# Kernel tuning notes

Hardware: AMD Instinct MI355X
Metric: run time of the kernel (lower is better)

The kernel has to match this reference:

```python
import jax, jax.numpy as jnp
import numpy as np

B, L, D, H, I = 4, 1024, 2048, 16, 8192
DH = D // H  # 128
EPS = 1e-6


def setup_inputs() -> dict:
    key = jax.random.key(0)
    ks = jax.random.split(key, 10)
    hidden_states = jax.random.normal(ks[0], (B, L, D), dtype=jnp.float32)
    # additive causal mask [B,1,L,L]: 0 on allowed, large negative on masked
    causal = jnp.tril(jnp.ones((L, L), dtype=bool))
    attention_mask = jnp.where(causal, 0.0, -1e9).astype(jnp.float32)
    attention_mask = jnp.broadcast_to(attention_mask[None, None], (B, 1, L, L))
    # RoPE tables [B,L,DH]
    inv_freq = 1.0 / (10000.0 ** (jnp.arange(0, DH, 2, dtype=jnp.float32) / DH))
    pos = jnp.arange(L, dtype=jnp.float32)
    freqs = pos[:, None] * inv_freq[None, :]            # [L, DH/2]
    emb = jnp.concatenate([freqs, freqs], axis=-1)       # [L, DH]
    cos = jnp.broadcast_to(jnp.cos(emb)[None], (B, L, DH)).astype(jnp.float32)
    sin = jnp.broadcast_to(jnp.sin(emb)[None], (B, L, DH)).astype(jnp.float32)
    s = 0.02
    return {
        "hidden_states": hidden_states,
        "attention_mask": attention_mask,
        "cos": cos,
        "sin": sin,
        "q_w": jax.random.normal(ks[1], (D, D), jnp.float32) * s,
        "k_w": jax.random.normal(ks[2], (D, D), jnp.float32) * s,
        "v_w": jax.random.normal(ks[3], (D, D), jnp.float32) * s,
        "o_w": jax.random.normal(ks[4], (D, D), jnp.float32) * s,
        "gate_w": jax.random.normal(ks[5], (I, D), jnp.float32) * s,
        "up_w": jax.random.normal(ks[6], (I, D), jnp.float32) * s,
        "down_w": jax.random.normal(ks[7], (D, I), jnp.float32) * s,
        "ln1_w": jnp.ones((D,), jnp.float32),
        "ln2_w": jnp.ones((D,), jnp.float32),
    }


def _rms_norm(x, w):
    var = jnp.mean(jnp.square(x), axis=-1, keepdims=True)
    return x * jax.lax.rsqrt(var + EPS) * w


def _rotate_half(x):
    x1, x2 = jnp.split(x, 2, axis=-1)
    return jnp.concatenate([-x2, x1], axis=-1)


def reference(hidden_states, attention_mask, cos, sin, q_w, k_w, v_w, o_w,
              gate_w, up_w, down_w, ln1_w, ln2_w):
    residual = hidden_states
    h = _rms_norm(hidden_states, ln1_w)                       # [B,L,D]
    # QKV projections (torch Linear: x @ W^T)
    def heads(x, w):
        return (x @ w.T).reshape(B, L, H, DH).transpose(0, 2, 1, 3)  # [B,H,L,DH]
    q, k, v = heads(h, q_w), heads(h, k_w), heads(h, v_w)
    cos_b, sin_b = cos[:, None], sin[:, None]                 # [B,1,L,DH]
    q = q * cos_b + _rotate_half(q) * sin_b
    k = k * cos_b + _rotate_half(k) * sin_b
    scores = jnp.einsum('bhqd,bhkd->bhqk', q, k) / jnp.sqrt(jnp.float32(DH))
    scores = scores + attention_mask                          # [B,H,L,L]
    attn = jax.nn.softmax(scores, axis=-1)
    ctx = jnp.einsum('bhqk,bhkd->bhqd', attn, v)              # [B,H,L,DH]
    ctx = ctx.transpose(0, 2, 1, 3).reshape(B, L, D)
    attn_out = ctx @ o_w.T
    h1 = residual + attn_out
    h2 = _rms_norm(h1, ln2_w)
    mlp = (jax.nn.silu(h2 @ gate_w.T) * (h2 @ up_w.T)) @ down_w.T
    out = h1 + mlp
    return out, attn
```

## Files before the change

### kernel.cpp

```cpp
#include <hip/hip_runtime.h>


typedef __bf16 bf16;
typedef __bf16 bf16x8 __attribute__((ext_vector_type(8)));
typedef __bf16 bf16x4 __attribute__((ext_vector_type(4)));
typedef float  f32x4  __attribute__((ext_vector_type(4)));

constexpr int   kB  = 4;
constexpr int   kL  = 1024;
constexpr int   kD  = 2048;
constexpr int   kH  = 16;
constexpr int   kI  = 8192;
constexpr int   kDH = 128;
constexpr int   kQKV = 3 * kD;
constexpr float kEps = 1e-6f;
constexpr float kScoreScale = 0.08838834764831845f;

typedef __attribute__((address_space(1))) void gvoid_t;
typedef __attribute__((address_space(3))) void lvoid_t;

__device__ __forceinline__ void gload_lds16(const void* g, void* l) {
  __builtin_amdgcn_global_load_lds((gvoid_t*)g, (lvoid_t*)l, 16, 0, 0);
}

#define ASM_VMCNT(n) asm volatile("s_waitcnt vmcnt(" #n ")" ::: "memory")

__device__ __forceinline__ void bar_raw() {
  asm volatile("" ::: "memory");
  __builtin_amdgcn_s_barrier();
  asm volatile("" ::: "memory");
}

__global__ __launch_bounds__(256) void cast_f32_bf16_kernel(
    const float* __restrict__ x, bf16* __restrict__ y, long n) {
  long i = ((long)blockIdx.x * 256 + threadIdx.x) * 4;
  long stride = (long)gridDim.x * 256 * 4;
  for (; i < n; i += stride) {
    const float4 v = *reinterpret_cast<const float4*>(x + i);
    bf16x4 o;
    o[0] = (bf16)v.x; o[1] = (bf16)v.y; o[2] = (bf16)v.z; o[3] = (bf16)v.w;
    *reinterpret_cast<bf16x4*>(y + i) = o;
  }
}

__global__ __launch_bounds__(256) void rmsnorm_kernel(
    const float* __restrict__ x, const float* __restrict__ w,
    bf16* __restrict__ out) {
  const long row = blockIdx.x;
  const float* xr = x + row * (long)kD;
  bf16* orow = out + row * (long)kD;
  const int t = threadIdx.x;

  float4 v0 = *(const float4*)(xr + t * 8);
  float4 v1 = *(const float4*)(xr + t * 8 + 4);
  float ss = v0.x * v0.x + v0.y * v0.y + v0.z * v0.z + v0.w * v0.w +
             v1.x * v1.x + v1.y * v1.y + v1.z * v1.z + v1.w * v1.w;

  __shared__ float red[4];
  for (int off = 32; off > 0; off >>= 1) ss += __shfl_down(ss, off);
  if ((t & 63) == 0) red[t >> 6] = ss;
  __syncthreads();
  const float tot = red[0] + red[1] + red[2] + red[3];
  const float rs = rsqrtf(tot / (float)kD + kEps);

  float4 w0 = *(const float4*)(w + t * 8);
  float4 w1 = *(const float4*)(w + t * 8 + 4);
  bf16x8 o;
  o[0] = (bf16)(v0.x * rs * w0.x); o[1] = (bf16)(v0.y * rs * w0.y);
  o[2] = (bf16)(v0.z * rs * w0.z); o[3] = (bf16)(v0.w * rs * w0.w);
  o[4] = (bf16)(v1.x * rs * w1.x); o[5] = (bf16)(v1.y * rs * w1.y);
  o[6] = (bf16)(v1.z * rs * w1.z); o[7] = (bf16)(v1.w * rs * w1.w);
  *(bf16x8*)(orow + t * 8) = o;
}

__global__ __launch_bounds__(256) void rope_kernel(
    bf16* __restrict__ qkv, const float* __restrict__ cosb,
    const float* __restrict__ sinb) {
  const long row = blockIdx.x;
  const float* cr = cosb + row * (long)kDH;
  const float* sr = sinb + row * (long)kDH;
  bf16* qr = qkv + row * (long)kQKV;
  bf16* kr = qr + kD;
  const int t = threadIdx.x;
#pragma unroll
  for (int it = 0; it < 4; ++it) {
    const int p = it * 256 + t;
    const int h = p >> 6, i = p & 63;
    const int i0 = h * kDH + i, i1 = i0 + 64;
    const float c0 = cr[i], s0 = sr[i], c1 = cr[i + 64], s1 = sr[i + 64];
    const float q0 = (float)qr[i0], q1 = (float)qr[i1];
    qr[i0] = (bf16)(q0 * c0 - q1 * s0);
    qr[i1] = (bf16)(q1 * c1 + q0 * s1);
    const float k0 = (float)kr[i0], k1 = (float)kr[i1];
    kr[i0] = (bf16)(k0 * c0 - k1 * s0);
    kr[i1] = (bf16)(k1 * c1 + k0 * s1);
  }
}

__global__ __launch_bounds__(256) void transpose_v_kernel(
    const bf16* __restrict__ qkv, bf16* __restrict__ vT) {
  __shared__ bf16 tile[32][33];
  const int z = blockIdx.z, b = z / kH, h = z % kH;
  const bf16* src = qkv + (long)b * kL * kQKV + 2 * kD + h * kDH;
  bf16* dst = vT + (long)z * kDH * kL;
  const int l0 = blockIdx.x * 32, d0 = blockIdx.y * 32;
  const int tx = threadIdx.x & 31, ty = threadIdx.x >> 5;
  for (int r = ty; r < 32; r += 8)
    tile[r][tx] = src[(long)(l0 + r) * kQKV + d0 + tx];
  __syncthreads();
  for (int r = ty; r < 32; r += 8)
    dst[(long)(d0 + r) * kL + l0 + tx] = tile[tx][r];
}

__global__ __launch_bounds__(256) void merge_stats_kernel(
    const float2* __restrict__ sp, float2* __restrict__ sm) {
  const int idx = blockIdx.x * 256 + threadIdx.x;
  const int row = idx & 1023;
  const int n = ((row >> 7) + 1) * 2;
  const float2* p = sp + ((long)idx << 4);
  float M = -3.0e38f;
  for (int i = 0; i < n; ++i) M = fmaxf(M, p[i].x);
  float S = 0.f;
  for (int i = 0; i < n; ++i) S += p[i].y * expf(p[i].x - M);
  sm[idx] = make_float2(M, 1.0f / S);
}

template <int EPI>
__global__ __launch_bounds__(512) void gemm256_body(
    const bf16* __restrict__ A, int lda, const bf16* __restrict__ B, int ldb,
    bf16* __restrict__ C, int ldc, const bf16* __restrict__ Ep, int lde,
    int K) {
  constexpr int NBUF = 3;
  __shared__ __align__(16) bf16 lsA[NBUF][256 * 32];
  __shared__ __align__(16) bf16 lsB[NBUF][256 * 32];

  const int t = threadIdx.x;
  const int m0 = blockIdx.x * 256, n0 = blockIdx.y * 256;
  const int wave = t >> 6, lane = t & 63;
  const int wm = (wave >> 2) * 128, wn = (wave & 3) * 64;
  const int lr = lane & 15, lg = lane >> 4;

  f32x4 acc[8][4] = {};

  auto stage = [&](int buf, int k0) {
#pragma unroll
    for (int c = 0; c < 2; ++c) {
      const int id = c * 512 + t;
      const int row = id >> 2, col = (id & 3) * 8;
      gload_lds16(A + (long)(m0 + row) * lda + k0 + col, &lsA[buf][id * 8]);
      gload_lds16(B + (long)(n0 + row) * ldb + k0 + col, &lsB[buf][id * 8]);
    }
  };

  auto compute = [&](int buf) {
    bf16x8 af[8], bfr[4];
#pragma unroll
    for (int i = 0; i < 8; ++i)
      af[i] = *(const bf16x8*)&lsA[buf][(wm + i * 16 + lr) * 32 + lg * 8];
#pragma unroll
    for (int j = 0; j < 4; ++j)
      bfr[j] = *(const bf16x8*)&lsB[buf][(wn + j * 16 + lr) * 32 + lg * 8];
#pragma unroll
    for (int i = 0; i < 8; ++i)
#pragma unroll
      for (int j = 0; j < 4; ++j)
        acc[i][j] = __builtin_amdgcn_mfma_f32_16x16x32_bf16(af[i], bfr[j],
                                                            acc[i][j], 0, 0, 0);
  };

  stage(0, 0);
  stage(1, 32);
  int cur = 0, k0 = 0;
  for (; k0 + 64 < K; k0 += 32) {
    const int nxt = cur == 2 ? 0 : cur + 1;
    const int pre = nxt == 2 ? 0 : nxt + 1;
    stage(pre, k0 + 64);
    ASM_VMCNT(8);
    bar_raw();
    compute(cur);
    bar_raw();
    cur = nxt;
  }
  ASM_VMCNT(4);
  bar_raw();
  compute(cur);
  cur = cur == 2 ? 0 : cur + 1;
  ASM_VMCNT(0);
  bar_raw();
  compute(cur);

#pragma unroll
  for (int i = 0; i < 8; ++i) {
#pragma unroll
    for (int j = 0; j < 4; ++j) {
      const int col = n0 + wn + j * 16 + lr;
#pragma unroll
      for (int r = 0; r < 4; ++r) {
        const int row = m0 + wm + i * 16 + lg * 4 + r;
        float val = acc[i][j][r];
        if constexpr (EPI == 3) {
          const float g = (float)Ep[(long)row * lde + col];
          val = (g / (1.0f + expf(-g))) * val;
        }
        C[(long)row * ldc + col] = (bf16)val;
      }
    }
  }
}

enum { EPI_NONE = 0, EPI_ADD = 1, EPI_OUTADD = 4, EPI_PASS1 = 6, EPI_PASS2 = 7 };

template <typename OutT, int EPI, bool AF32, int NF, bool CK>
__device__ __forceinline__ void gemm_body(
    const void* __restrict__ Ap, long sAo, long sAi, int lda,
    const bf16* __restrict__ Bp, long sBo, long sBi, int ldb,
    OutT* Cp, long sCo, long sCi, int ldc,
    const void* Ep, long sEo, long sEi, int lde,
    float scale, int Hdiv, int M, int N, int K) {
  constexpr int BN = 32 * NF;
  constexpr int ACH = 512;
  constexpr int BCH = BN * 4;
  static_assert((EPI != EPI_PASS1 && EPI != EPI_PASS2) || NF == 4, "pass NF=4");

  const int z = blockIdx.z;
  const int zo = z / Hdiv, zi = z % Hdiv;

  const bf16* A = nullptr;
  const float* Af = nullptr;
  if constexpr (AF32) Af = (const float*)Ap + zo * sAo + zi * sAi;
  else                A  = (const bf16*)Ap + zo * sAo + zi * sAi;
  const bf16* Bw = Bp + zo * sBo + zi * sBi;
  OutT* C = Cp + zo * sCo + zi * sCi;

  const int t = threadIdx.x;
  const int m0 = blockIdx.y * 128, n0 = blockIdx.x * BN;

  if constexpr (EPI == EPI_PASS1) {
    if (blockIdx.x > blockIdx.y) return;
  }
  if constexpr (EPI == EPI_PASS2) {
    if (blockIdx.x > blockIdx.y) {
      for (int e = t; e < 128 * 32; e += 256) {
        const int row = e >> 5, col = (e & 31) * 4;
        *(float4*)&C[(long)(m0 + row) * ldc + n0 + col] =
            make_float4(0.f, 0.f, 0.f, 0.f);
      }
      return;
    }
  }

  __shared__ __align__(16) bf16 lsA[2][128 * 32];
  __shared__ __align__(16) bf16 lsB[2][BN * 32];

  const int wave = t >> 6, lane = t & 63;
  const int wm = (wave >> 1) * 64, wn = (wave & 1) * (NF * 16);
  const int lr = lane & 15, lg = lane >> 4;

  f32x4 acc[4][NF] = {};

  auto stage = [&](int buf, int k0) {
    if constexpr (AF32) {
#pragma unroll
      for (int c = 0; c < 2; ++c) {
        const int id = c * 256 + t;
        const int row = id >> 2, col = (id & 3) * 8;
        const float* src = Af + (long)(m0 + row) * lda + k0 + col;
        const float4 u0 = *(const float4*)src;
        const float4 u1 = *(const float4*)(src + 4);
        bf16x8 wv;
        wv[0] = (bf16)u0.x; wv[1] = (bf16)u0.y; wv[2] = (bf16)u0.z; wv[3] = (bf16)u0.w;
        wv[4] = (bf16)u1.x; wv[5] = (bf16)u1.y; wv[6] = (bf16)u1.z; wv[7] = (bf16)u1.w;
        *(bf16x8*)&lsA[buf][id * 8] = wv;
        if (NF == 4 || c == 0)
          gload_lds16(Bw + (long)(n0 + row) * ldb + k0 + col, &lsB[buf][id * 8]);
      }
    } else {
#pragma unroll
      for (int c = 0; c < (ACH + BCH) / 256; ++c) {
        const int id = c * 256 + t;
        if (id < ACH) {
          const int row = id >> 2, col = (id & 3) * 8;
          gload_lds16(A + (long)(m0 + row) * lda + k0 + col, &lsA[buf][id * 8]);
        } else {
          const int fid = id - ACH;
          const int row = fid >> 2, col = (fid & 3) * 8;
          gload_lds16(Bw + (long)(n0 + row) * ldb + k0 + col, &lsB[buf][fid * 8]);
        }
      }
    }
  };

  auto compute = [&](int buf) {
    bf16x8 af[4], bfr[NF];
#pragma unroll
    for (int i = 0; i < 4; ++i)
      af[i] = *(const bf16x8*)&lsA[buf][(wm + i * 16 + lr) * 32 + lg * 8];
#pragma unroll
    for (int j = 0; j < NF; ++j)
      bfr[j] = *(const bf16x8*)&lsB[buf][(wn + j * 16 + lr) * 32 + lg * 8];
#pragma unroll
    for (int i = 0; i < 4; ++i)
#pragma unroll
      for (int j = 0; j < NF; ++j)
        acc[i][j] = __builtin_amdgcn_mfma_f32_16x16x32_bf16(af[i], bfr[j],
                                                            acc[i][j], 0, 0, 0);
  };

  const int Klim = CK ? (m0 + 128) : K;
  int cur = 0;

  if constexpr (AF32) {
    stage(0, 0);
    __syncthreads();
    for (int k0 = 0; k0 < Klim - 32; k0 += 32) {
      stage(cur ^ 1, k0 + 32);
      compute(cur);
      __syncthreads();
      cur ^= 1;
    }
    compute(cur);
  } else {
    stage(0, 0);
    for (int k0 = 0; k0 < Klim - 32; k0 += 32) {
      stage(cur ^ 1, k0 + 32);
      if constexpr (NF == 4) ASM_VMCNT(4); else ASM_VMCNT(3);
      bar_raw();
      compute(cur);
      bar_raw();
      cur ^= 1;
    }
    ASM_VMCNT(0);
    bar_raw();
    compute(cur);
  }

  if constexpr (EPI == EPI_PASS1) {
    float2* statsP = (float2*)Ep;
    const int half = wn >> 6, nt = blockIdx.x;
#pragma unroll
    for (int i = 0; i < 4; ++i) {
#pragma unroll
      for (int r = 0; r < 4; ++r) {
        const int rowg = m0 + wm + i * 16 + lg * 4 + r;
        float v[NF];
        float mx = -3.0e38f;
#pragma unroll
        for (int j = 0; j < NF; ++j) {
          const int colg = n0 + wn + j * 16 + lr;
          v[j] = acc[i][j][r] * scale + (colg > rowg ? -1.0e9f : 0.0f);
          mx = fmaxf(mx, v[j]);
        }
        for (int sh = 1; sh <= 8; sh <<= 1) mx = fmaxf(mx, __shfl_xor(mx, sh));
        float s = 0.f;
#pragma unroll
        for (int j = 0; j < NF; ++j) s += expf(v[j] - mx);
        for (int sh = 1; sh <= 8; sh <<= 1) s += __shfl_xor(s, sh);
        if (lr == 0)
          statsP[(((long)(z << 10) + rowg) << 4) + nt * 2 + half] =
              make_float2(mx, s);
      }
    }
  } else if constexpr (EPI == EPI_PASS2) {
    const float2* sm = (const float2*)Ep;
#pragma unroll
    for (int i = 0; i < 4; ++i) {
#pragma unroll
      for (int j = 0; j < NF; ++j) {
        const int colg = n0 + wn + j * 16 + lr;
#pragma unroll
        for (int r = 0; r < 4; ++r) {
          const int rowg = m0 + wm + i * 16 + lg * 4 + r;
          float p = 0.0f;
          if (colg <= rowg) {
            const float2 st = sm[(z << 10) + rowg];
            p = expf(acc[i][j][r] * scale - st.x) * st.y;
          }
          C[(long)rowg * ldc + colg] = (OutT)p;
        }
      }
    }
  } else {
    const float* Ef = (const float*)Ep;
    long ebase = 0;
    if constexpr (EPI == EPI_ADD)
      ebase = zo * sEo + zi * sEi;
#pragma unroll
    for (int i = 0; i < 4; ++i) {
#pragma unroll
      for (int j = 0; j < NF; ++j) {
        const int col = n0 + wn + j * 16 + lr;
#pragma unroll
        for (int r = 0; r < 4; ++r) {
          const int rowi = m0 + wm + i * 16 + lg * 4 + r;
          float val = acc[i][j][r] * scale;
          const long idx = (long)rowi * ldc + col;
          if constexpr (EPI == EPI_ADD)
            val += Ef[ebase + (long)rowi * lde + col];
          if constexpr (EPI == EPI_OUTADD)
            val += (float)C[idx];
          C[idx] = (OutT)val;
        }
      }
    }
  }
}

#define GEMM_ARGS                                                        \
  const void* __restrict__ Ap, long sAo, long sAi, int lda,              \
  const bf16* __restrict__ Bp, long sBo, long sBi, int ldb,              \
  void* Cp, long sCo, long sCi, int ldc,                                 \
  const void* Ep, long sEo, long sEi, int lde,                           \
  float scale, int Hdiv, int M, int N, int K
#define GEMM_PASS Ap, sAo, sAi, lda, Bp, sBo, sBi, ldb, (OUT_T*)Cp, sCo, \
  sCi, ldc, Ep, sEo, sEi, lde, scale, Hdiv, M, N, K

#define DEF_GEMM(NAME, OUT_TY, EPI_V, AF32_V, NF_V, CK_V)                \
  __global__ __launch_bounds__(256) void NAME(GEMM_ARGS) {               \
    using OUT_T = OUT_TY;                                                \
    gemm_body<OUT_T, EPI_V, AF32_V, NF_V, CK_V>(GEMM_PASS);              \
  }

DEF_GEMM(gemm_sc1,   float, EPI_PASS1,  false, 4, false)
DEF_GEMM(gemm_sc2,   float, EPI_PASS2,  false, 4, false)
DEF_GEMM(gemm_ctx,   bf16,  EPI_NONE,   true,  2, true)
DEF_GEMM(gemm_oproj, float, EPI_ADD,    false, 2, false)
DEF_GEMM(gemm_down,  float, EPI_OUTADD, false, 2, false)

extern "C" void kernel_launch(void* const* d_in, const int* in_sizes, int n_in,
                              void* d_out, int out_size, void* d_ws,
                              size_t ws_size, hipStream_t stream) {
  (void)in_sizes; (void)n_in; (void)out_size; (void)ws_size;

  const float* hidden = (const float*)d_in[0];
  const float* cosb   = (const float*)d_in[2];
  const float* sinb   = (const float*)d_in[3];
  const float* q_w    = (const float*)d_in[4];
  const float* k_w    = (const float*)d_in[5];
  const float* v_w    = (const float*)d_in[6];
  const float* o_w    = (const float*)d_in[7];
  const float* gate_w = (const float*)d_in[8];
  const float* up_w   = (const float*)d_in[9];
  const float* down_w = (const float*)d_in[10];
  const float* ln1    = (const float*)d_in[11];
  const float* ln2    = (const float*)d_in[12];

  float* out  = (float*)d_out;
  float* attn = out + (long)kB * kL * kD;

  bf16* wsb = (bf16*)d_ws;
  long off = 0;
  bf16* WQKV = wsb + off; off += 3L * kD * kD;
  bf16* WO   = wsb + off; off += (long)kD * kD;
  bf16* WBIG = wsb + off; off += (long)kI * kD;
  bf16* HBF  = wsb + off; off += (long)kB * kL * kD;
  bf16* QKV  = wsb + off; off += (long)kB * kL * kQKV;
  bf16* GBUF = wsb + off; off += (long)kB * kL * kI;

  float2* STATS_P = (float2*)HBF;
  float2* STATS_M = STATS_P + (64L * 1024 * 16);

  const long DD = (long)kD * kD;
  const long ID = (long)kI * kD;
  const int  ML = kB * kL;

  cast_f32_bf16_kernel<<<dim3((int)(DD / 1024)), 256, 0, stream>>>(q_w, WQKV, DD);
  cast_f32_bf16_kernel<<<dim3((int)(DD / 1024)), 256, 0, stream>>>(k_w, WQKV + DD, DD);
  cast_f32_bf16_kernel<<<dim3((int)(DD / 1024)), 256, 0, stream>>>(v_w, WQKV + 2 * DD, DD);
  cast_f32_bf16_kernel<<<dim3((int)(DD / 1024)), 256, 0, stream>>>(o_w, WO, DD);

  rmsnorm_kernel<<<ML, 256, 0, stream>>>(hidden, ln1, HBF);

  gemm256_body<0><<<dim3(ML / 256, kQKV / 256), 512, 0, stream>>>(
      HBF, kD, WQKV, kD, QKV, kQKV, nullptr, 0, kD);

  rope_kernel<<<ML, 256, 0, stream>>>(QKV, cosb, sinb);

  transpose_v_kernel<<<dim3(kL / 32, kDH / 32, kB * kH), 256, 0, stream>>>(QKV, GBUF);

  gemm_sc1<<<dim3(kL / 128, kL / 128, kB * kH), 256, 0, stream>>>(
      QKV, (long)kL * kQKV, kDH, kQKV,
      QKV + kD, (long)kL * kQKV, kDH, kQKV,
      attn, (long)kH * kL * kL, (long)kL * kL, kL,
      STATS_P, 0, 0, 0,
      kScoreScale, kH, kL, kL, kDH);

  merge_stats_kernel<<<256, 256, 0, stream>>>(STATS_P, STATS_M);

  gemm_sc2<<<dim3(kL / 128, kL / 128, kB * kH), 256, 0, stream>>>(
      QKV, (long)kL * kQKV, kDH, kQKV,
      QKV + kD, (long)kL * kQKV, kDH, kQKV,
      attn, (long)kH * kL * kL, (long)kL * kL, kL,
      STATS_M, 0, 0, 0,
      kScoreScale, kH, kL, kL, kDH);

  gemm_ctx<<<dim3(kDH / 64, kL / 128, kB * kH), 256, 0, stream>>>(
      attn, (long)kH * kL * kL, (long)kL * kL, kL,
      GBUF, (long)kH * kDH * kL, (long)kDH * kL, kL,
      HBF, (long)kL * kD, kDH, kD,
      nullptr, 0, 0, 0, 1.0f, kH, kL, kDH, kL);

  gemm_oproj<<<dim3(kD / 64, ML / 128, 1), 256, 0, stream>>>(
      HBF, 0, 0, kD, WO, 0, 0, kD, out, 0, 0, kD,
      hidden, 0, 0, kD, 1.0f, 1, ML, kD, kD);

  bf16* H2 = QKV;
  rmsnorm_kernel<<<ML, 256, 0, stream>>>(out, ln2, H2);

  cast_f32_bf16_kernel<<<dim3((int)(ID / 1024)), 256, 0, stream>>>(gate_w, WBIG, ID);
  gemm256_body<0><<<dim3(ML / 256, kI / 256), 512, 0, stream>>>(
      H2, kD, WBIG, kD, GBUF, kI, nullptr, 0, kD);

  cast_f32_bf16_kernel<<<dim3((int)(ID / 1024)), 256, 0, stream>>>(up_w, WBIG, ID);
  gemm256_body<3><<<dim3(ML / 256, kI / 256), 512, 0, stream>>>(
      H2, kD, WBIG, kD, GBUF, kI, GBUF, kI, kD);

  cast_f32_bf16_kernel<<<dim3((int)(ID / 1024)), 256, 0, stream>>>(down_w, WBIG, ID);
  gemm_down<<<dim3(kD / 64, ML / 128, 1), 256, 0, stream>>>(
      GBUF, 0, 0, kI, WBIG, 0, 0, kI, out, 0, 0, kD,
      nullptr, 0, 0, 0, 1.0f, 1, ML, kD, kI);
}
```

Baseline: 1.143 ms.

## Rewrite 256x256 GEMM with BK=64 XOR-swizzled LDS and phased prefetch

```diff
diff --git a/kernel.cpp b/kernel.cpp
--- a/kernel.cpp
+++ b/kernel.cpp
@@ -126,78 +126,99 @@
 }
 
 template <int EPI>
-__global__ __launch_bounds__(512) void gemm256_body(
+__global__ __launch_bounds__(512) void gemm8p(
     const bf16* __restrict__ A, int lda, const bf16* __restrict__ B, int ldb,
     bf16* __restrict__ C, int ldc, const bf16* __restrict__ Ep, int lde,
     int K) {
-  constexpr int NBUF = 3;
-  __shared__ __align__(16) bf16 lsA[NBUF][256 * 32];
-  __shared__ __align__(16) bf16 lsB[NBUF][256 * 32];
-
+  __shared__ __align__(16) bf16 ls[2][2][2][128 * 64];
   const int t = threadIdx.x;
   const int m0 = blockIdx.x * 256, n0 = blockIdx.y * 256;
   const int wave = t >> 6, lane = t & 63;
-  const int wm = (wave >> 2) * 128, wn = (wave & 3) * 64;
+  const int ah = wave >> 2;
+  const int wm = ah * 128;
+  const int wn = (wave & 3) * 64;
+  const int bh = wn >> 7;
+  const int wnr = wn & 127;
   const int lr = lane & 15, lg = lane >> 4;
 
   f32x4 acc[8][4] = {};
 
-  auto stage = [&](int buf, int k0) {
-#pragma unroll
-    for (int c = 0; c < 2; ++c) {
-      const int id = c * 512 + t;
-      const int row = id >> 2, col = (id & 3) * 8;
-      gload_lds16(A + (long)(m0 + row) * lda + k0 + col, &lsA[buf][id * 8]);
-      gload_lds16(B + (long)(n0 + row) * ldb + k0 + col, &lsB[buf][id * 8]);
+  auto stageHalf = [&](int b, int O, int h, int k0) {
+    const bf16* S = O ? B : A;
+    const int ld = O ? ldb : lda;
+    const int base = O ? n0 : m0;
+#pragma unroll
+    for (int cc = 0; cc < 2; ++cc) {
+      const int id = cc * 512 + t;
+      const int row = id >> 3, cS = id & 7;
+      const int cG = cS ^ (row & 7);
+      gload_lds16(S + (long)(base + h * 128 + row) * ld + k0 + cG * 8,
+                  (char*)&ls[b][O][h][0] + id * 16);
     }
   };
 
-  auto compute = [&](int buf) {
-    bf16x8 af[8], bfr[4];
-#pragma unroll
-    for (int i = 0; i < 8; ++i)
-      af[i] = *(const bf16x8*)&lsA[buf][(wm + i * 16 + lr) * 32 + lg * 8];
-#pragma unroll
-    for (int j = 0; j < 4; ++j)
-      bfr[j] = *(const bf16x8*)&lsB[buf][(wn + j * 16 + lr) * 32 + lg * 8];
-#pragma unroll
-    for (int i = 0; i < 8; ++i)
-#pragma unroll
-      for (int j = 0; j < 4; ++j)
-        acc[i][j] = __builtin_amdgcn_mfma_f32_16x16x32_bf16(af[i], bfr[j],
-                                                            acc[i][j], 0, 0, 0);
+  auto lread = [&](int b, int O, int h, int row, int c16) {
+    return *(const bf16x8*)((const char*)&ls[b][O][h][0] + row * 128 +
+                            ((c16 ^ (row & 7)) << 4));
   };
 
-  stage(0, 0);
-  stage(1, 32);
-  int cur = 0, k0 = 0;
-  for (; k0 + 64 < K; k0 += 32) {
-    const int nxt = cur == 2 ? 0 : cur + 1;
-    const int pre = nxt == 2 ? 0 : nxt + 1;
-    stage(pre, k0 + 64);
-    ASM_VMCNT(8);
-    bar_raw();
-    compute(cur);
-    bar_raw();
-    cur = nxt;
-  }
-  ASM_VMCNT(4);
-  bar_raw();
-  compute(cur);
-  cur = cur == 2 ? 0 : cur + 1;
-  ASM_VMCNT(0);
-  bar_raw();
-  compute(cur);
-
-#pragma unroll
-  for (int i = 0; i < 8; ++i) {
-#pragma unroll
-    for (int j = 0; j < 4; ++j) {
-      const int col = n0 + wn + j * 16 + lr;
+  const int T = K >> 6;
+  stageHalf(0, 0, 0, 0); stageHalf(0, 0, 1, 0);
+  stageHalf(0, 1, 0, 0); stageHalf(0, 1, 1, 0);
+  stageHalf(1, 1, 0, 64); stageHalf(1, 1, 1, 64);
+
+  bf16x8 bfr[2][4];
+
+  for (int w = 0; w < T; ++w) {
+    const int c = w & 1;
+    const int k1 = (w + 1) << 6, k2 = (w + 2) << 6;
+#pragma unroll
+    for (int p = 0; p < 4; ++p) {
+      bf16x8 af[2][2];
+      if (p == 0) {
+        if (w + 1 < T) { ASM_VMCNT(4); } else { ASM_VMCNT(0); }
+        bar_raw();
+#pragma unroll
+        for (int kk = 0; kk < 2; ++kk)
+#pragma unroll
+          for (int nf = 0; nf < 4; ++nf)
+            bfr[kk][nf] = lread(c, 1, bh, wnr + nf * 16 + lr, kk * 4 + lg);
+      }
+#pragma unroll
+      for (int kk = 0; kk < 2; ++kk)
+#pragma unroll
+        for (int mf = 0; mf < 2; ++mf)
+          af[kk][mf] = lread(c, 0, ah, (2 * p + mf) * 16 + lr, kk * 4 + lg);
+      if (p == 0 && w + 1 < T) stageHalf(c ^ 1, 0, 0, k1);
+      if (p == 1 && w + 1 < T) stageHalf(c ^ 1, 0, 1, k1);
+      if (p == 2 && w + 2 < T) stageHalf(c, 1, 0, k2);
+      if (p == 3 && w + 2 < T) stageHalf(c, 1, 1, k2);
+      bar_raw();
+      asm volatile("s_waitcnt lgkmcnt(0)" ::: "memory");
+      __builtin_amdgcn_sched_barrier(0);
+      __builtin_amdgcn_s_setprio(1);
+#pragma unroll
+      for (int kk = 0; kk < 2; ++kk)
+#pragma unroll
+        for (int mf = 0; mf < 2; ++mf)
+#pragma unroll
+          for (int nf = 0; nf < 4; ++nf)
+            acc[2 * p + mf][nf] = __builtin_amdgcn_mfma_f32_16x16x32_bf16(
+                af[kk][mf], bfr[kk][nf], acc[2 * p + mf][nf], 0, 0, 0);
+      __builtin_amdgcn_s_setprio(0);
+      bar_raw();
+    }
+  }
+
+#pragma unroll
+  for (int mf = 0; mf < 8; ++mf) {
+#pragma unroll
+    for (int nf = 0; nf < 4; ++nf) {
+      const int col = n0 + wn + nf * 16 + lr;
 #pragma unroll
       for (int r = 0; r < 4; ++r) {
-        const int row = m0 + wm + i * 16 + lg * 4 + r;
-        float val = acc[i][j][r];
+        const int row = m0 + wm + mf * 16 + lg * 4 + r;
+        float val = acc[mf][nf][r];
         if constexpr (EPI == 3) {
           const float g = (float)Ep[(long)row * lde + col];
           val = (g / (1.0f + expf(-g))) * val;
@@ -470,7 +491,7 @@
 
   rmsnorm_kernel<<<ML, 256, 0, stream>>>(hidden, ln1, HBF);
 
-  gemm256_body<0><<<dim3(ML / 256, kQKV / 256), 512, 0, stream>>>(
+  gemm8p<0><<<dim3(ML / 256, kQKV / 256), 512, 0, stream>>>(
       HBF, kD, WQKV, kD, QKV, kQKV, nullptr, 0, kD);
 
   rope_kernel<<<ML, 256, 0, stream>>>(QKV, cosb, sinb);
@@ -507,11 +528,11 @@
   rmsnorm_kernel<<<ML, 256, 0, stream>>>(out, ln2, H2);
 
   cast_f32_bf16_kernel<<<dim3((int)(ID / 1024)), 256, 0, stream>>>(gate_w, WBIG, ID);
-  gemm256_body<0><<<dim3(ML / 256, kI / 256), 512, 0, stream>>>(
+  gemm8p<0><<<dim3(ML / 256, kI / 256), 512, 0, stream>>>(
       H2, kD, WBIG, kD, GBUF, kI, nullptr, 0, kD);
 
   cast_f32_bf16_kernel<<<dim3((int)(ID / 1024)), 256, 0, stream>>>(up_w, WBIG, ID);
-  gemm256_body<3><<<dim3(ML / 256, kI / 256), 512, 0, stream>>>(
+  gemm8p<3><<<dim3(ML / 256, kI / 256), 512, 0, stream>>>(
       H2, kD, WBIG, kD, GBUF, kI, GBUF, kI, kD);
 
   cast_f32_bf16_kernel<<<dim3((int)(ID / 1024)), 256, 0, stream>>>(down_w, WBIG, ID);
```

Result: faster. 1.076 ms (-5.9%).
